# Kernel tuning notes

Hardware: AMD Instinct MI355X
Metric: run time of the kernel (lower is better)

The kernel has to match this reference:

```python
import jax, jax.numpy as jnp
import numpy as np

SEQ, D_IN, D_OUT = 8192, 768, 64


def setup_inputs() -> dict:
    key = jax.random.key(0)
    kx, kq, kk, kv = jax.random.split(key, 4)
    scale = 1.0 / np.sqrt(D_IN)
    return {
        "x": jax.random.normal(kx, (SEQ, D_IN), dtype=jnp.float32),
        # torch Linear weight layout: [d_out, d_in]
        "W_Q": jax.random.uniform(kq, (D_OUT, D_IN), dtype=jnp.float32, minval=-scale, maxval=scale),
        "W_K": jax.random.uniform(kk, (D_OUT, D_IN), dtype=jnp.float32, minval=-scale, maxval=scale),
        "W_V": jax.random.uniform(kv, (D_OUT, D_IN), dtype=jnp.float32, minval=-scale, maxval=scale),
    }


def reference(x, W_Q, W_K, W_V):
    # q,k,v: [seq, d_out]
    q = x @ W_Q.T
    k = x @ W_K.T
    v = x @ W_V.T
    scores = (q @ k.T) / jnp.sqrt(jnp.asarray(k.shape[-1], x.dtype))  # [seq, seq]
    attn = jax.nn.softmax(scores, axis=-1)
    return attn @ v  # [seq, d_out]
```

## Files before the change

kernel.cpp:

```cpp
#include <hip/hip_runtime.h>
#include <hip/hip_bf16.h>
#include <math.h>

#define SEQ 8192
#define DIN 768
#define DOUT 64
#define QSCALE 0.1803368801111214f

typedef __attribute__((ext_vector_type(8))) short short8;
typedef __attribute__((ext_vector_type(4))) short short4v;
typedef __attribute__((ext_vector_type(4))) float floatx4;
typedef __attribute__((ext_vector_type(2))) unsigned int uint2v;

__device__ __forceinline__ void gload16(const void* g, void* l) {
    __builtin_amdgcn_global_load_lds(
        (const __attribute__((address_space(1))) unsigned int*)g,
        (__attribute__((address_space(3))) unsigned int*)l, 16, 0, 0);
}

__device__ __forceinline__ unsigned pack2(float a, float b) {
    __hip_bfloat162 h = __float22bfloat162_rn(make_float2(a, b));
    return *(unsigned*)&h;
}

__device__ __forceinline__ unsigned short bfbits(float f) {
    __hip_bfloat16 h = __float2bfloat16(f);
    return *(unsigned short*)&h;
}

__device__ __forceinline__ float bf2f(unsigned short u) {
    unsigned v = ((unsigned)u) << 16;
    return *(float*)&v;
}

__device__ __forceinline__ float exp2r(float x) {
#if __has_builtin(__builtin_amdgcn_exp2f)
    return __builtin_amdgcn_exp2f(x);
#else
    float r; asm("v_exp_f32 %0, %1" : "=v"(r) : "v"(x)); return r;
#endif
}

__device__ __forceinline__ floatx4 mfma16(short4v a, short4v b, floatx4 c) {
#if __has_builtin(__builtin_amdgcn_mfma_f32_16x16x16bf16_1k)
    return __builtin_amdgcn_mfma_f32_16x16x16bf16_1k(a, b, c, 0, 0, 0);
#else
    asm("v_mfma_f32_16x16x16_bf16 %0, %1, %2, %0" : "+v"(c) : "v"(a), "v"(b));
    return c;
#endif
}

#define BAR()       asm volatile("s_barrier" ::: "memory")
#define WAIT_VM4()  asm volatile("s_waitcnt vmcnt(4)" ::: "memory")
#define WAIT_VM0()  asm volatile("s_waitcnt vmcnt(0)" ::: "memory")

__global__ __launch_bounds__(512) void qkv_mfma(
    const float* __restrict__ x,
    const float* __restrict__ Wq, const float* __restrict__ Wk,
    const float* __restrict__ Wv,
    unsigned short* __restrict__ qbf, unsigned short* __restrict__ kbf,
    unsigned short* __restrict__ vtbf)
{
    __shared__ __align__(16) unsigned char xs[2][32 * 128];
    __shared__ __align__(16) unsigned char wsm[2][192 * 128];

    const int t = threadIdx.x;
    const int l = t & 63;
    const int wid = t >> 6;
    const int h = wid & 1;
    const int ntb = (wid >> 1) * 3;
    const int g = l >> 4;
    const int q4 = l & 15;
    const int row0 = blockIdx.x * 32;

    const int wrow0 = (t >> 3) * 3;
    const int wc8   = t & 7;
    const int xrow = t >> 4;
    const int xc4  = t & 15;

    float4 wreg[3][2];
    float4 xA, xB, x0;

#define WLOAD(k0)                                                             \
    {                                                                         \
        _Pragma("unroll")                                                     \
        for (int rr = 0; rr < 3; ++rr) {                                      \
            const int row = wrow0 + rr;                                       \
            const float* wp = (row < 64)  ? &Wq[(size_t)row * DIN]            \
                           : (row < 128) ? &Wk[(size_t)(row - 64) * DIN]      \
                                         : &Wv[(size_t)(row - 128) * DIN];    \
            wreg[rr][0] = *(const float4*)&wp[(k0) + wc8 * 8];                \
            wreg[rr][1] = *(const float4*)&wp[(k0) + wc8 * 8 + 4];            \
        }                                                                     \
    }
#define WWRITE(buf)                                                           \
    {                                                                         \
        _Pragma("unroll")                                                     \
        for (int rr = 0; rr < 3; ++rr) {                                      \
            const int row = wrow0 + rr;                                       \
            uint4 v;                                                          \
            v.x = pack2(wreg[rr][0].x, wreg[rr][0].y);                        \
            v.y = pack2(wreg[rr][0].z, wreg[rr][0].w);                        \
            v.z = pack2(wreg[rr][1].x, wreg[rr][1].y);                        \
            v.w = pack2(wreg[rr][1].z, wreg[rr][1].w);                        \
            *(uint4*)&wsm[buf][row * 128 + ((wc8 ^ (row & 7)) << 4)] = v;     \
        }                                                                     \
    }
#define XLOAD(dst, k0)                                                        \
    dst = *(const float4*)&x[(size_t)(row0 + xrow) * DIN + (k0) + xc4 * 4];
#define XWRITE(buf, src)                                                      \
    {                                                                         \
        uint2 v2;                                                             \
        v2.x = pack2(src.x, src.y);                                           \
        v2.y = pack2(src.z, src.w);                                           \
        const int half = xc4 & 1, slq = xc4 >> 1;                             \
        *(uint2*)&xs[buf][xrow * 128 + ((slq ^ (xrow & 7)) << 4) + half * 8] = v2; \
    }

    floatx4 acc[3];
#pragma unroll
    for (int i = 0; i < 3; ++i) acc[i] = (floatx4){0.f, 0.f, 0.f, 0.f};

    WLOAD(0)
    XLOAD(x0, 0)
    XLOAD(xA, 64)
    XLOAD(xB, 128)
    WWRITE(0)
    XWRITE(0, x0)
    WLOAD(64)
    __syncthreads();

#pragma unroll
    for (int kc = 0; kc < 12; ++kc) {
        const int cur = kc & 1;

        __builtin_amdgcn_s_setprio(1);
#pragma unroll
        for (int ks = 0; ks < 2; ++ks) {
            const int sl = g + 4 * ks;
            const int Rx = h * 16 + q4;
            const short8 a = *(const short8*)&xs[cur][Rx * 128 + ((sl ^ (Rx & 7)) << 4)];
#pragma unroll
            for (int j = 0; j < 3; ++j) {
                const int Rw = (ntb + j) * 16 + q4;
                const short8 b = *(const short8*)&wsm[cur][Rw * 128 + ((sl ^ (Rw & 7)) << 4)];
                acc[j] = __builtin_amdgcn_mfma_f32_16x16x32_bf16(a, b, acc[j], 0, 0, 0);
            }
        }
        __builtin_amdgcn_s_setprio(0);

        if (kc + 1 < 12) {
            WWRITE(cur ^ 1)
            if ((kc + 1) & 1) { XWRITE(cur ^ 1, xA) } else { XWRITE(cur ^ 1, xB) }
            if (kc + 2 < 12) WLOAD((kc + 2) * 64)
            if (kc + 3 < 12) {
                if ((kc + 3) & 1) { XLOAD(xA, (kc + 3) * 64) }
                else             { XLOAD(xB, (kc + 3) * 64) }
            }
        }
        __syncthreads();
    }

    const int rb = row0 + h * 16 + (g << 2);
#pragma unroll
    for (int j = 0; j < 3; ++j) {
        const int nt = ntb + j;
#pragma unroll
        for (int r = 0; r < 4; ++r) {
            const float v = acc[j][r];
            const int R = rb + r;
            if (nt < 4) {
                qbf[(size_t)R * 64 + nt * 16 + q4] = bfbits(v * QSCALE);
            } else if (nt < 8) {
                kbf[(size_t)R * 64 + (nt - 4) * 16 + q4] = bfbits(v);
            } else {
                vtbf[(size_t)((nt - 8) * 16 + q4) * SEQ + R] = bfbits(v);
            }
        }
    }
#undef WLOAD
#undef WWRITE
#undef XLOAD
#undef XWRITE
}

__global__ __launch_bounds__(256, 4) void flash_mfma(
    const unsigned short* __restrict__ qbf,
    const unsigned short* __restrict__ kbf,
    const unsigned short* __restrict__ vtbf,
    void* __restrict__ opart,
    float* __restrict__ ml,
    int nsplit, int direct)
{
    __shared__ __align__(16) unsigned char lds[32768];
    unsigned char* lkb = lds;
    unsigned char* lvb = lds + 16384;

    const int t = threadIdx.x;
    const int l = t & 63;
    const int g = l >> 4;
    const int q4 = l & 15;
    const int wid = t >> 6;
    const int row0 = blockIdx.x * 128;
    const int split = blockIdx.y;
    const int chunk = SEQ / nsplit;
    const int kbeg = split * chunk;
    const int NT = chunk / 64;

#define ISSUE_KV(buf, kt)                                                     \
    {                                                                         \
        const int Rr = l >> 3;                                                \
        const int sl = (l & 7) ^ Rr;                                          \
        _Pragma("unroll")                                                     \
        for (int ss = 0; ss < 2; ++ss) {                                      \
            const int s = wid * 2 + ss;                                       \
            const int R = 8 * s + Rr;                                         \
            gload16(&kbf[(size_t)((kt) + R) * 64 + sl * 8],                   \
                    lkb + (buf) * 8192 + s * 1024);                           \
            gload16(&vtbf[(size_t)R * SEQ + (kt) + sl * 8],                   \
                    lvb + (buf) * 8192 + s * 1024);                           \
        }                                                                     \
    }

    short8 qf[2][2];
#pragma unroll
    for (int qt = 0; qt < 2; ++qt)
#pragma unroll
        for (int ks = 0; ks < 2; ++ks)
            qf[qt][ks] = *(const short8*)&qbf[
                (size_t)(row0 + wid * 32 + qt * 16 + q4) * 64 + (g + 4 * ks) * 8];

    ISSUE_KV(0, kbeg)
    if (NT > 1) ISSUE_KV(1, kbeg + 64)

    floatx4 oacc[2][4];
#pragma unroll
    for (int i = 0; i < 2; ++i)
#pragma unroll
        for (int j = 0; j < 4; ++j) oacc[i][j] = (floatx4){0.f, 0.f, 0.f, 0.f};
    floatx4 l_acc[2] = {(floatx4){0.f, 0.f, 0.f, 0.f},
                        (floatx4){0.f, 0.f, 0.f, 0.f}};

    int cur = 0;
    for (int tt = 0; tt < NT; ++tt) {
        if (tt + 1 < NT) { WAIT_VM4(); } else { WAIT_VM0(); }
        BAR();

        const unsigned char* lk = lkb + cur * 8192;
        const unsigned char* lv = lvb + cur * 8192;

        floatx4 sacc[2][4];
#pragma unroll
        for (int i = 0; i < 2; ++i)
#pragma unroll
            for (int j = 0; j < 4; ++j) sacc[i][j] = (floatx4){0.f, 0.f, 0.f, 0.f};
        __builtin_amdgcn_s_setprio(1);
#pragma unroll
        for (int ks = 0; ks < 2; ++ks) {
            const int sl = g + 4 * ks;
#pragma unroll
            for (int nt = 0; nt < 4; ++nt) {
                const int R = nt * 16 + q4;
                const short8 kf = *(const short8*)&lk[R * 128 + ((sl ^ (R & 7)) << 4)];
                sacc[0][nt] = __builtin_amdgcn_mfma_f32_16x16x32_bf16(kf, qf[0][ks], sacc[0][nt], 0, 0, 0);
                sacc[1][nt] = __builtin_amdgcn_mfma_f32_16x16x32_bf16(kf, qf[1][ks], sacc[1][nt], 0, 0, 0);
            }
        }
        __builtin_amdgcn_s_setprio(0);

        floatx4 pv[2][4];
#pragma unroll
        for (int qt = 0; qt < 2; ++qt) {
#pragma unroll
            for (int nt = 0; nt < 4; ++nt) {
                pv[qt][nt][0] = exp2r(sacc[qt][nt][0]);
                pv[qt][nt][1] = exp2r(sacc[qt][nt][1]);
                pv[qt][nt][2] = exp2r(sacc[qt][nt][2]);
                pv[qt][nt][3] = exp2r(sacc[qt][nt][3]);
            }
            l_acc[qt] += (pv[qt][0] + pv[qt][1]) + (pv[qt][2] + pv[qt][3]);
        }

        __builtin_amdgcn_s_setprio(1);
#pragma unroll
        for (int kb = 0; kb < 4; ++kb) {
            const short4v pb0 = __builtin_bit_cast(short4v,
                (uint2v){pack2(pv[0][kb][0], pv[0][kb][1]),
                         pack2(pv[0][kb][2], pv[0][kb][3])});
            const short4v pb1 = __builtin_bit_cast(short4v,
                (uint2v){pack2(pv[1][kb][0], pv[1][kb][1]),
                         pack2(pv[1][kb][2], pv[1][kb][3])});
            const int sl = kb * 2 + (g >> 1);
#pragma unroll
            for (int dt = 0; dt < 4; ++dt) {
                const int R = dt * 16 + q4;
                const short4v a = *(const short4v*)&lv[R * 128 +
                    ((sl ^ (R & 7)) << 4) + ((g & 1) << 3)];
                oacc[0][dt] = mfma16(a, pb0, oacc[0][dt]);
                oacc[1][dt] = mfma16(a, pb1, oacc[1][dt]);
            }
        }
        __builtin_amdgcn_s_setprio(0);

        BAR();
        if (tt + 2 < NT) ISSUE_KV(cur, kbeg + (tt + 2) * 64)
        cur ^= 1;
    }

    float l_run[2];
#pragma unroll
    for (int qt = 0; qt < 2; ++qt) {
        float s = (l_acc[qt][0] + l_acc[qt][1]) + (l_acc[qt][2] + l_acc[qt][3]);
        s += __shfl_xor(s, 16);
        s += __shfl_xor(s, 32);
        l_run[qt] = s;
    }

    if (!direct && g == 0) {
#pragma unroll
        for (int qt = 0; qt < 2; ++qt) {
            const size_t mrow = (size_t)split * SEQ + row0 + wid * 32 + qt * 16 + q4;
            ml[mrow * 2 + 0] = 0.0f;
            ml[mrow * 2 + 1] = l_run[qt];
        }
    }

    if (direct) {
        float* trans = (float*)lds;
        float* outbase = (float*)opart;
#pragma unroll
        for (int qt = 0; qt < 2; ++qt) {
            __syncthreads();
            {
                const int r = wid * 16 + q4;
                const float sc = 1.0f / l_run[qt];
#pragma unroll
                for (int dt = 0; dt < 4; ++dt)
                    *(floatx4*)&trans[r * 68 + dt * 16 + g * 4] = oacc[qt][dt] * sc;
            }
            __syncthreads();
#pragma unroll
            for (int it = 0; it < 4; ++it) {
                const int r = it * 16 + (t >> 4);
                const int qrow = row0 + ((r >> 4) << 5) + qt * 16 + (r & 15);
                const floatx4 v = *(const floatx4*)&trans[r * 68 + (t & 15) * 4];
                *(floatx4*)&outbase[(size_t)qrow * 64 + (t & 15) * 4] = v;
            }
        }
    } else {
        unsigned short* transb = (unsigned short*)lds;
        unsigned short* outb = (unsigned short*)opart + (size_t)split * SEQ * 64;
#pragma unroll
        for (int qt = 0; qt < 2; ++qt) {
            __syncthreads();
            {
                const int r = wid * 16 + q4;
#pragma unroll
                for (int dt = 0; dt < 4; ++dt) {
                    uint2 v2;
                    v2.x = pack2(oacc[qt][dt][0], oacc[qt][dt][1]);
                    v2.y = pack2(oacc[qt][dt][2], oacc[qt][dt][3]);
                    *(uint2*)&transb[r * 72 + dt * 16 + g * 4] = v2;
                }
            }
            __syncthreads();
#pragma unroll
            for (int it = 0; it < 2; ++it) {
                const int r = it * 32 + (t >> 3);
                const int qrow = row0 + ((r >> 4) << 5) + qt * 16 + (r & 15);
                const short8 v = *(const short8*)&transb[r * 72 + (t & 7) * 8];
                *(short8*)&outb[(size_t)qrow * 64 + (t & 7) * 8] = v;
            }
        }
    }
#undef ISSUE_KV
}

__global__ __launch_bounds__(256) void combine_kernel(
    const unsigned short* __restrict__ opart, const float* __restrict__ ml,
    float* __restrict__ out, int nsplit)
{
    const int i8 = (blockIdx.x * 256 + threadIdx.x) * 8;
    if (i8 >= SEQ * DOUT) return;
    const int row = i8 >> 6;

    float denom = 0.f;
    float acc[8] = {0.f, 0.f, 0.f, 0.f, 0.f, 0.f, 0.f, 0.f};
    for (int s = 0; s < nsplit; ++s) {
        denom += ml[((size_t)s * SEQ + row) * 2 + 1];
        const short8 v = *(const short8*)&opart[(size_t)s * SEQ * DOUT + i8];
#pragma unroll
        for (int j = 0; j < 8; ++j)
            acc[j] += bf2f((unsigned short)v[j]);
    }
    const float inv = 1.0f / denom;
    floatx4 o0 = {acc[0] * inv, acc[1] * inv, acc[2] * inv, acc[3] * inv};
    floatx4 o1 = {acc[4] * inv, acc[5] * inv, acc[6] * inv, acc[7] * inv};
    *(floatx4*)&out[i8] = o0;
    *(floatx4*)&out[i8 + 4] = o1;
}

extern "C" void kernel_launch(void* const* d_in, const int* in_sizes, int n_in,
                              void* d_out, int out_size, void* d_ws, size_t ws_size,
                              hipStream_t stream)
{
    const float* x  = (const float*)d_in[0];
    const float* Wq = (const float*)d_in[1];
    const float* Wk = (const float*)d_in[2];
    const float* Wv = (const float*)d_in[3];
    float* out = (float*)d_out;
    unsigned char* ws = (unsigned char*)d_ws;

    const size_t qkv_b = (size_t)SEQ * 64 * 2;
    size_t off = 0;
    unsigned short* qbf  = (unsigned short*)(ws + off); off += qkv_b;
    unsigned short* kbf  = (unsigned short*)(ws + off); off += qkv_b;
    unsigned short* vtbf = (unsigned short*)(ws + off); off += qkv_b;

    const size_t per_split = (size_t)SEQ * 64 * 2 + (size_t)SEQ * 2 * 4;
    int nsplit = 0;
    if      (ws_size >= off + 16 * per_split) nsplit = 16;
    else if (ws_size >= off + 8 * per_split)  nsplit = 8;
    else if (ws_size >= off + 4 * per_split)  nsplit = 4;
    else if (ws_size >= off + 2 * per_split)  nsplit = 2;

    qkv_mfma<<<SEQ / 32, 512, 0, stream>>>(x, Wq, Wk, Wv, qbf, kbf, vtbf);

    if (nsplit == 0) {
        flash_mfma<<<dim3(SEQ / 128, 1), 256, 0, stream>>>(
            qbf, kbf, vtbf, (void*)out, nullptr, 1, 1);
    } else {
        unsigned short* opart = (unsigned short*)(ws + off);
        float* mlp = (float*)(ws + off + (size_t)nsplit * SEQ * 64 * 2);
        flash_mfma<<<dim3(SEQ / 128, nsplit), 256, 0, stream>>>(
            qbf, kbf, vtbf, (void*)opart, mlp, nsplit, 0);
        combine_kernel<<<SEQ * DOUT / 8 / 256, 256, 0, stream>>>(
            opart, mlp, out, nsplit);
    }
}
```

Baseline: 53.14 us.

## Pre-convert weights to bf16 and stream them into LDS via async global_load_lds

Adds a small prep kernel that converts the three fp32 weight matrices to one packed bf16 buffer. The QKV projection kernel now moves each W tile straight into LDS with global_load_lds, which avoids the per-block fp32 load, convert and LDS write. It halves the block size to 256 threads, with each wave computing six output tiles instead of three. Synchronisation switches to explicit vmcnt waits and barriers. The cost is an extra kernel launch, plus fewer waves per block that may hide less latency.

```diff
diff --git a/kernel.cpp b/kernel.cpp
--- a/kernel.cpp
+++ b/kernel.cpp
@@ -51,13 +51,36 @@
 }
 
 #define BAR()       asm volatile("s_barrier" ::: "memory")
+#define CFENCE()    asm volatile("" ::: "memory")
+#define WAIT_VM8()  asm volatile("s_waitcnt vmcnt(8)" ::: "memory")
+#define WAIT_VM6()  asm volatile("s_waitcnt vmcnt(6)" ::: "memory")
 #define WAIT_VM4()  asm volatile("s_waitcnt vmcnt(4)" ::: "memory")
 #define WAIT_VM0()  asm volatile("s_waitcnt vmcnt(0)" ::: "memory")
-
-__global__ __launch_bounds__(512) void qkv_mfma(
-    const float* __restrict__ x,
+#define WAIT_LGKM() asm volatile("s_waitcnt lgkmcnt(0)" ::: "memory")
+
+__global__ __launch_bounds__(256) void prep_w(
     const float* __restrict__ Wq, const float* __restrict__ Wk,
-    const float* __restrict__ Wv,
+    const float* __restrict__ Wv, unsigned short* __restrict__ wbf)
+{
+    const int i = blockIdx.x * 256 + threadIdx.x;
+    const int base = i * 8;
+    const int row = base / DIN;
+    const int k = base % DIN;
+    const float* src = (row < 64)  ? &Wq[(size_t)row * DIN + k]
+                     : (row < 128) ? &Wk[(size_t)(row - 64) * DIN + k]
+                                   : &Wv[(size_t)(row - 128) * DIN + k];
+    const float4 f0 = *(const float4*)src;
+    const float4 f1 = *(const float4*)(src + 4);
+    uint4 v;
+    v.x = pack2(f0.x, f0.y);
+    v.y = pack2(f0.z, f0.w);
+    v.z = pack2(f1.x, f1.y);
+    v.w = pack2(f1.z, f1.w);
+    *(uint4*)&wbf[base] = v;
+}
+
+__global__ __launch_bounds__(256) void qkv_mfma(
+    const float* __restrict__ x, const unsigned short* __restrict__ wbf,
     unsigned short* __restrict__ qbf, unsigned short* __restrict__ kbf,
     unsigned short* __restrict__ vtbf)
 {
@@ -68,71 +91,63 @@
     const int l = t & 63;
     const int wid = t >> 6;
     const int h = wid & 1;
-    const int ntb = (wid >> 1) * 3;
+    const int ntb = (wid >> 1) * 6;
     const int g = l >> 4;
     const int q4 = l & 15;
     const int row0 = blockIdx.x * 32;
 
-    const int wrow0 = (t >> 3) * 3;
-    const int wc8   = t & 7;
-    const int xrow = t >> 4;
-    const int xc4  = t & 15;
-
-    float4 wreg[3][2];
-    float4 xA, xB, x0;
-
-#define WLOAD(k0)                                                             \
+    const int Rx_st = t >> 3;
+    const int slx   = t & 7;
+    const int Rr    = l >> 3;
+    const int sld   = (l & 7) ^ Rr;
+
+    floatx4 acc[6];
+#pragma unroll
+    for (int i = 0; i < 6; ++i) acc[i] = (floatx4){0.f, 0.f, 0.f, 0.f};
+
+#define ISSUE_W(buf, k0)                                                      \
     {                                                                         \
         _Pragma("unroll")                                                     \
-        for (int rr = 0; rr < 3; ++rr) {                                      \
-            const int row = wrow0 + rr;                                       \
-            const float* wp = (row < 64)  ? &Wq[(size_t)row * DIN]            \
-                           : (row < 128) ? &Wk[(size_t)(row - 64) * DIN]      \
-                                         : &Wv[(size_t)(row - 128) * DIN];    \
-            wreg[rr][0] = *(const float4*)&wp[(k0) + wc8 * 8];                \
-            wreg[rr][1] = *(const float4*)&wp[(k0) + wc8 * 8 + 4];            \
+        for (int ss = 0; ss < 6; ++ss) {                                      \
+            const int s = wid * 6 + ss;                            \
+            const int Rw = 8 * s + Rr;                            \
+            gload16(&wbf[(size_t)Rw * DIN + (k0) + sld * 8], &wsm[buf][s * 1024]); \
         }                                                                     \
     }
-#define WWRITE(buf)                                                           \
+#define LOAD_X(da, db, k0)                                                    \
     {                                                                         \
-        _Pragma("unroll")                                                     \
-        for (int rr = 0; rr < 3; ++rr) {                                      \
-            const int row = wrow0 + rr;                                       \
-            uint4 v;                                                          \
-            v.x = pack2(wreg[rr][0].x, wreg[rr][0].y);                        \
-            v.y = pack2(wreg[rr][0].z, wreg[rr][0].w);                        \
-            v.z = pack2(wreg[rr][1].x, wreg[rr][1].y);                        \
-            v.w = pack2(wreg[rr][1].z, wreg[rr][1].w);                        \
-            *(uint4*)&wsm[buf][row * 128 + ((wc8 ^ (row & 7)) << 4)] = v;     \
-        }                                                                     \
-    }
-#define XLOAD(dst, k0)                                                        \
-    dst = *(const float4*)&x[(size_t)(row0 + xrow) * DIN + (k0) + xc4 * 4];
-#define XWRITE(buf, src)                                                      \
+        da = *(const float4*)&x[(size_t)(row0 + Rx_st) * DIN + (k0) + slx * 8];     \
+        db = *(const float4*)&x[(size_t)(row0 + Rx_st) * DIN + (k0) + slx * 8 + 4]; \
+    }
+#define WRITE_X(buf, sa, sb)                                                  \
     {                                                                         \
-        uint2 v2;                                                             \
-        v2.x = pack2(src.x, src.y);                                           \
-        v2.y = pack2(src.z, src.w);                                           \
-        const int half = xc4 & 1, slq = xc4 >> 1;                             \
-        *(uint2*)&xs[buf][xrow * 128 + ((slq ^ (xrow & 7)) << 4) + half * 8] = v2; \
-    }
-
-    floatx4 acc[3];
-#pragma unroll
-    for (int i = 0; i < 3; ++i) acc[i] = (floatx4){0.f, 0.f, 0.f, 0.f};
-
-    WLOAD(0)
-    XLOAD(x0, 0)
-    XLOAD(xA, 64)
-    XLOAD(xB, 128)
-    WWRITE(0)
-    XWRITE(0, x0)
-    WLOAD(64)
-    __syncthreads();
+        uint4 v;                                                              \
+        v.x = pack2(sa.x, sa.y); v.y = pack2(sa.z, sa.w);                     \
+        v.z = pack2(sb.x, sb.y); v.w = pack2(sb.z, sb.w);                     \
+        *(uint4*)&xs[buf][Rx_st * 128 + ((slx ^ (Rx_st & 7)) << 4)] = v;      \
+    }
+
+    float4 xAa, xAb;
+    float4 xBa, xBb;
+    {
+        float4 a0, b0;
+        ISSUE_W(0, 0)
+        LOAD_X(a0, b0, 0)
+        CFENCE();
+        ISSUE_W(1, 64)
+        LOAD_X(xAa, xAb, 64)
+        LOAD_X(xBa, xBb, 128)
+        WRITE_X(0, a0, b0)
+    }
 
 #pragma unroll
     for (int kc = 0; kc < 12; ++kc) {
         const int cur = kc & 1;
+        if (kc <= 9)       { WAIT_VM8(); }
+        else if (kc == 10) { WAIT_VM6(); }
+        else               { WAIT_VM0(); }
+        WAIT_LGKM();
+        BAR();
 
         __builtin_amdgcn_s_setprio(1);
 #pragma unroll
@@ -141,29 +156,29 @@
             const int Rx = h * 16 + q4;
             const short8 a = *(const short8*)&xs[cur][Rx * 128 + ((sl ^ (Rx & 7)) << 4)];
 #pragma unroll
-            for (int j = 0; j < 3; ++j) {
+            for (int j = 0; j < 6; ++j) {
                 const int Rw = (ntb + j) * 16 + q4;
                 const short8 b = *(const short8*)&wsm[cur][Rw * 128 + ((sl ^ (Rw & 7)) << 4)];
                 acc[j] = __builtin_amdgcn_mfma_f32_16x16x32_bf16(a, b, acc[j], 0, 0, 0);
             }
         }
         __builtin_amdgcn_s_setprio(0);
+        BAR();
 
         if (kc + 1 < 12) {
-            WWRITE(cur ^ 1)
-            if ((kc + 1) & 1) { XWRITE(cur ^ 1, xA) } else { XWRITE(cur ^ 1, xB) }
-            if (kc + 2 < 12) WLOAD((kc + 2) * 64)
+            if (kc + 2 < 12) ISSUE_W(cur, (kc + 2) * 64)
+            if ((kc + 1) & 1) { WRITE_X(cur ^ 1, xAa, xAb) }
+            else              { WRITE_X(cur ^ 1, xBa, xBb) }
             if (kc + 3 < 12) {
-                if ((kc + 3) & 1) { XLOAD(xA, (kc + 3) * 64) }
-                else             { XLOAD(xB, (kc + 3) * 64) }
-            }
-        }
-        __syncthreads();
+                if ((kc + 3) & 1) { LOAD_X(xAa, xAb, (kc + 3) * 64) }
+                else              { LOAD_X(xBa, xBb, (kc + 3) * 64) }
+            }
+        }
     }
 
     const int rb = row0 + h * 16 + (g << 2);
 #pragma unroll
-    for (int j = 0; j < 3; ++j) {
+    for (int j = 0; j < 6; ++j) {
         const int nt = ntb + j;
 #pragma unroll
         for (int r = 0; r < 4; ++r) {
@@ -178,10 +193,9 @@
             }
         }
     }
-#undef WLOAD
-#undef WWRITE
-#undef XLOAD
-#undef XWRITE
+#undef ISSUE_W
+#undef LOAD_X
+#undef WRITE_X
 }
 
 __global__ __launch_bounds__(256, 4) void flash_mfma(
@@ -411,8 +425,10 @@
     float* out = (float*)d_out;
     unsigned char* ws = (unsigned char*)d_ws;
 
+    const size_t wbf_b = (size_t)192 * DIN * 2;
     const size_t qkv_b = (size_t)SEQ * 64 * 2;
     size_t off = 0;
+    unsigned short* wbf  = (unsigned short*)(ws + off); off += wbf_b;
     unsigned short* qbf  = (unsigned short*)(ws + off); off += qkv_b;
     unsigned short* kbf  = (unsigned short*)(ws + off); off += qkv_b;
     unsigned short* vtbf = (unsigned short*)(ws + off); off += qkv_b;
@@ -424,7 +440,8 @@
     else if (ws_size >= off + 4 * per_split)  nsplit = 4;
     else if (ws_size >= off + 2 * per_split)  nsplit = 2;
 
-    qkv_mfma<<<SEQ / 32, 512, 0, stream>>>(x, Wq, Wk, Wv, qbf, kbf, vtbf);
+    prep_w<<<72, 256, 0, stream>>>(Wq, Wk, Wv, wbf);
+    qkv_mfma<<<SEQ / 32, 256, 0, stream>>>(x, wbf, qbf, kbf, vtbf);
 
     if (nsplit == 0) {
         flash_mfma<<<dim3(SEQ / 128, 1), 256, 0, stream>>>(
```

New measurement: 57.19 us. 1.08x slower.
